# Optimization experiments

Measured on AMD Instinct MI355X. Metric: run time of the kernel, lower is better.

## Reference

```python
import jax, jax.numpy as jnp
import numpy as np
from jax import lax

B, C, H, L = 4, 64, 8, 2048  # batch, per-head channels, heads, sequence length


def setup_inputs() -> dict:
    key = jax.random.key(0)
    ks = jax.random.split(key, 15)

    def p(k, shape, s=0.05):
        return jax.random.normal(k, shape, jnp.float32) * s

    inp = {"x": jax.random.normal(ks[0], (B, C, L), jnp.float32)}
    for i, nm in enumerate(["q", "k", "v"]):
        inp[f"{nm}_dw"] = p(ks[1 + 4 * i], (C, 1, 3))       # depthwise conv weight, groups=C, k=3
        inp[f"{nm}_db"] = p(ks[2 + 4 * i], (C,))
        inp[f"{nm}_pw"] = p(ks[3 + 4 * i], (H * C, C))      # pointwise 1x1 conv weight
        inp[f"{nm}_pb"] = p(ks[4 + 4 * i], (H * C,))
    inp["u_w"] = p(ks[13], (C, H * C))                      # unify_heads 1x1 conv weight
    inp["u_b"] = p(ks[14], (C,))
    return inp


def dsconv(x, dw, db, pw, pb):
    # Depth-separable conv1d: depthwise (k=3, pad=1, groups=C) then pointwise 1x1.
    c = x.shape[1]
    y = lax.conv_general_dilated(x, dw, window_strides=(1,), padding=[(1, 1)],
                                 dimension_numbers=("NCH", "OIH", "NCH"),
                                 feature_group_count=c)
    y = y + db[None, :, None]
    return jnp.einsum("bcl,oc->bol", y, pw) + pb[None, :, None]


def reference(x, q_dw, q_db, q_pw, q_pb, k_dw, k_db, k_pw, k_pb,
              v_dw, v_db, v_pw, v_pb, u_w, u_b):
    b, c, l = x.shape
    h = H
    scale = c ** (-0.25)
    q = dsconv(x, q_dw, q_db, q_pw, q_pb).reshape(b, h, c, l) * scale
    k = dsconv(x, k_dw, k_db, k_pw, k_pb).reshape(b, h, c, l) * scale
    v = dsconv(x, v_dw, v_db, v_pw, v_pb).reshape(b, h, c, l)
    # dot[b,h,i,j] = sum_c k[b,h,c,i] * q[b,h,c,j]  (i = key pos, j = query pos)
    dot = jnp.einsum("bhci,bhcj->bhij", k, q)
    att = jax.nn.softmax(dot, axis=2)  # normalize over key positions (torch dim=1 of [bh,l,l])
    out = jnp.einsum("bhci,bhij->bhcj", v, att).reshape(b, h * c, l)
    return jnp.einsum("bkl,ck->bcl", out, u_w) + u_b[None, :, None]
```

## Files before the change

### kernel.cpp

```cpp
#include <hip/hip_runtime.h>
#include <hip/hip_bf16.h>
#include <stdint.h>
#include <string.h>

typedef unsigned short u16;
typedef unsigned int u32;
typedef __bf16 bf16x8 __attribute__((ext_vector_type(8)));
typedef float f32x4 __attribute__((ext_vector_type(4)));

#define NB 4
#define NC 64
#define NH 8
#define NL 2048
#define HC 512

#define XT_OFF  ((size_t)0)
#define WM_OFF  ((size_t)1 << 20)
#define PBM_OFF ((size_t)2 << 20)
#define V_OFF   ((size_t)4 << 20)
#define QT_OFF  ((size_t)12 << 20)
#define KT_OFF  ((size_t)20 << 20)

#define LP 72

#if __has_builtin(__builtin_amdgcn_exp2f)
#define EXP2F __builtin_amdgcn_exp2f
#else
#define EXP2F exp2f
#endif

static __device__ __forceinline__ u16 f2bfu(float f) {
  union { float f; unsigned int i; } x; x.f = f;
  unsigned int i = x.i;
  return (u16)((i + 0x7fffu + ((i >> 16) & 1u)) >> 16);
}
static __device__ __forceinline__ u32 pk2(float a, float b) {
  float2 f; f.x = a; f.y = b;
  __hip_bfloat162 h = __float22bfloat162_rn(f);
  u32 w; __builtin_memcpy(&w, &h, 4); return w;
}
static __device__ __forceinline__ bf16x8 ld_bf8(const u16* p) {
  bf16x8 v; __builtin_memcpy(&v, p, 16); return v;
}

__global__ __launch_bounds__(256) void init_out(
    const float* __restrict__ ub, float* __restrict__ out)
{
  int i4 = blockIdx.x * 256 + threadIdx.x;
  int c = (i4 >> 9) & 63;
  float f = ub[c];
  float4 v = {f, f, f, f};
  ((float4*)out)[i4] = v;
}

__global__ __launch_bounds__(256) void prep_w(
    const float* __restrict__ qdw, const float* __restrict__ qdb,
    const float* __restrict__ qpw, const float* __restrict__ qpb,
    const float* __restrict__ kdw, const float* __restrict__ kdb,
    const float* __restrict__ kpw, const float* __restrict__ kpb,
    const float* __restrict__ vdw, const float* __restrict__ vdb,
    const float* __restrict__ vpw, const float* __restrict__ vpb,
    u16* __restrict__ Wm, float* __restrict__ pbm)
{
  int idx = blockIdx.x * 256 + threadIdx.x;
  if (idx < 98304) {
    int tns = idx >> 15, r = idx & 32767, o = r >> 6, c = r & 63;
    const float* dw = (tns == 0) ? qdw : (tns == 1) ? kdw : vdw;
    const float* pw = (tns == 0) ? qpw : (tns == 1) ? kpw : vpw;
    float s = (tns == 0) ? 0.35355339059327373f * 1.4426950408889634f
            : (tns == 1) ? 0.35355339059327373f : 1.0f;
    float w = pw[o * 64 + c] * s;
#pragma unroll
    for (int d = 0; d < 3; ++d)
      Wm[((size_t)(tns * 3 + d) * 512 + o) * 64 + c] = f2bfu(w * dw[c * 3 + d]);
  } else if (idx < 98304 + 1536) {
    int i = idx - 98304;
    int tns = i >> 9, o = i & 511;
    const float* db = (tns == 0) ? qdb : (tns == 1) ? kdb : vdb;
    const float* pw = (tns == 0) ? qpw : (tns == 1) ? kpw : vpw;
    const float* pb = (tns == 0) ? qpb : (tns == 1) ? kpb : vpb;
    float s = (tns == 0) ? 0.35355339059327373f * 1.4426950408889634f
            : (tns == 1) ? 0.35355339059327373f : 1.0f;
    float bias = pb[o];
    for (int c = 0; c < 64; ++c) bias += pw[o * 64 + c] * db[c];
    pbm[i] = bias * s;
  }
}

__global__ __launch_bounds__(256) void prep_x(
    const float* __restrict__ x, u16* __restrict__ xT)
{
  __shared__ __align__(16) u16 T[64 * LP];
  int bx = blockIdx.x;
  int lt = bx & 31, b = bx >> 5;
  int tid = threadIdx.x;
  {
    int c = tid & 63, ls = (tid >> 6) * 16;
    const float4* g = (const float4*)(x + ((size_t)b * NC + c) * NL + lt * 64 + ls);
    u16 tmp[16];
#pragma unroll
    for (int j4 = 0; j4 < 4; ++j4) {
      float4 f = g[j4];
      tmp[j4*4+0] = f2bfu(f.x); tmp[j4*4+1] = f2bfu(f.y);
      tmp[j4*4+2] = f2bfu(f.z); tmp[j4*4+3] = f2bfu(f.w);
    }
#pragma unroll
    for (int j = 0; j < 16; ++j) T[(ls + j) * LP + c] = tmp[j];
  }
  __syncthreads();
  {
    int r = tid >> 2, cs = (tid & 3) * 16;
    uint4 a = *(const uint4*)&T[r * LP + cs];
    uint4 b2 = *(const uint4*)&T[r * LP + cs + 8];
    u16* o = xT + ((size_t)b * NL + lt * 64 + r) * 64 + cs;
    *(uint4*)o = a;
    *(uint4*)(o + 8) = b2;
  }
}

__global__ __launch_bounds__(256) void qkv_gemm(
    const u16* __restrict__ xT, const u16* __restrict__ Wm,
    const float* __restrict__ pbm,
    u16* __restrict__ v, u16* __restrict__ qT, u16* __restrict__ kT)
{
  __shared__ __align__(16) u16 WS[3][64 * LP];
  __shared__ __align__(16) u16 XS[66 * LP];

  int bx = blockIdx.x;
  int och = bx & 7;
  int tns = (bx >> 3) % 3;
  int rest = bx / 24;
  int lt = rest & 31, b = rest >> 5;

  int tid = threadIdx.x;
  int wave = tid >> 6, lane = tid & 63, quad = lane >> 4, l16 = lane & 15;

  {
    const u16* wg = Wm + ((size_t)(tns * 3) * 512 + och * 64) * 64;
    for (int s = tid; s < 1536; s += 256) {
      int d = s >> 9, r = s & 511;
      int o = r >> 3, c4 = r & 7;
      uint4 w = *(const uint4*)(wg + ((size_t)d * 512 + o) * 64 + c4 * 8);
      *(uint4*)&WS[d][o * LP + c4 * 8] = w;
    }
  }
  {
    const u16* xg = xT + (size_t)b * NL * 64;
    int l0m1 = lt * 64 - 1;
    for (int s = tid; s < 528; s += 256) {
      int r = s >> 3, c4 = s & 7;
      int g = l0m1 + r;
      uint4 w = {0, 0, 0, 0};
      if ((unsigned)g < (unsigned)NL) w = *(const uint4*)(xg + (size_t)g * 64 + c4 * 8);
      *(uint4*)&XS[r * LP + c4 * 8] = w;
    }
  }
  __syncthreads();

  f32x4 acc[4] = {{0,0,0,0},{0,0,0,0},{0,0,0,0},{0,0,0,0}};

  if (tns == 2) {
    bf16x8 aw[3][2];
#pragma unroll
    for (int d = 0; d < 3; ++d)
#pragma unroll
      for (int kh = 0; kh < 2; ++kh)
        aw[d][kh] = ld_bf8(&WS[d][(wave * 16 + l16) * LP + kh * 32 + quad * 8]);
#pragma unroll
    for (int nt = 0; nt < 4; ++nt)
#pragma unroll
      for (int d = 0; d < 3; ++d)
#pragma unroll
        for (int kh = 0; kh < 2; ++kh) {
          bf16x8 bx8 = ld_bf8(&XS[(nt * 16 + l16 + d) * LP + kh * 32 + quad * 8]);
          acc[nt] = __builtin_amdgcn_mfma_f32_16x16x32_bf16(aw[d][kh], bx8, acc[nt], 0, 0, 0);
        }
  } else {
    bf16x8 ax[3][2];
#pragma unroll
    for (int d = 0; d < 3; ++d)
#pragma unroll
      for (int kh = 0; kh < 2; ++kh)
        ax[d][kh] = ld_bf8(&XS[(wave * 16 + l16 + d) * LP + kh * 32 + quad * 8]);
#pragma unroll
    for (int nt = 0; nt < 4; ++nt)
#pragma unroll
      for (int d = 0; d < 3; ++d)
#pragma unroll
        for (int kh = 0; kh < 2; ++kh) {
          bf16x8 bw = ld_bf8(&WS[d][(nt * 16 + l16) * LP + kh * 32 + quad * 8]);
          acc[nt] = __builtin_amdgcn_mfma_f32_16x16x32_bf16(ax[d][kh], bw, acc[nt], 0, 0, 0);
        }
  }

  __syncthreads();
  u16* OS = &WS[0][0];

  if (tns == 2) {
    const float* pbt = pbm + tns * 512 + och * 64 + wave * 16;
#pragma unroll
    for (int nt = 0; nt < 4; ++nt)
#pragma unroll
      for (int rr = 0; rr < 4; ++rr)
        OS[(wave * 16 + quad * 4 + rr) * LP + nt * 16 + l16] =
            f2bfu(acc[nt][rr] + pbt[quad * 4 + rr]);
  } else {
    const float* pbt = pbm + tns * 512 + och * 64;
#pragma unroll
    for (int nt = 0; nt < 4; ++nt) {
      float bias = pbt[nt * 16 + l16];
#pragma unroll
      for (int rr = 0; rr < 4; ++rr)
        OS[(wave * 16 + quad * 4 + rr) * LP + nt * 16 + l16] = f2bfu(acc[nt][rr] + bias);
    }
  }
  __syncthreads();

  {
    int r = tid >> 2, ck = (tid & 3) * 16;
    uint4 a = *(const uint4*)&OS[r * LP + ck];
    uint4 b2 = *(const uint4*)&OS[r * LP + ck + 8];
    u16* gp;
    if (tns == 2)
      gp = v + ((size_t)(b * HC + och * 64 + r)) * NL + lt * 64 + ck;
    else {
      u16* dst = (tns == 0) ? qT : kT;
      gp = dst + ((size_t)(b * 8 + och) * NL + lt * 64 + r) * 64 + ck;
    }
    *(uint4*)gp = a;
    *(uint4*)(gp + 8) = b2;
  }
}

__global__ __launch_bounds__(256) void attn_kernel(
    const u16* __restrict__ qT, const u16* __restrict__ kT,
    const u16* __restrict__ vg, const float* __restrict__ uw,
    float* __restrict__ outg)
{
  __shared__ __align__(16) u16 Kt[64 * LP];
  __shared__ __align__(16) u16 Vt[64 * LP];
  __shared__ __align__(16) u16 UW[64 * LP];
  __shared__ __align__(16) u16 QP[128 * LP];

  int bx = blockIdx.x;
  int qt = bx & 15, bh = bx >> 4;
  int b = bh >> 3, h = bh & 7;
  int tid = threadIdx.x;
  int wave = tid >> 6, lane = tid & 63, quad = lane >> 4, l16 = lane & 15;

  const u16* Qh = qT + (size_t)bh * NL * 64;
  const u16* Kh = kT + (size_t)bh * NL * 64;
  const u16* Vh = vg + ((size_t)(b * HC + h * NC)) * NL;
  int q0 = qt * 128;

  int sr = tid >> 2, ss = (tid & 3) * 16;
  int vc = tid & 63, vk = (tid >> 6) * 16;

  {
    int r = tid >> 1, cs = (tid & 1) * 32;
    const u16* g = Qh + (size_t)(q0 + r) * 64 + cs;
    uint4 a0 = *(const uint4*)g;
    uint4 a1 = *(const uint4*)(g + 8);
    uint4 a2 = *(const uint4*)(g + 16);
    uint4 a3 = *(const uint4*)(g + 24);
    u16* d = &QP[r * LP + cs];
    *(uint4*)d = a0; *(uint4*)(d + 8) = a1;
    *(uint4*)(d + 16) = a2; *(uint4*)(d + 24) = a3;
  }
  {
    int c = tid >> 2, g = (tid & 3) * 16;
    const float4* s = (const float4*)(uw + (size_t)c * HC + h * 64 + g);
#pragma unroll
    for (int j = 0; j < 4; ++j) {
      float4 w = s[j];
      u16* d = &UW[c * LP + g + j * 4];
      d[0] = f2bfu(w.x); d[1] = f2bfu(w.y); d[2] = f2bfu(w.z); d[3] = f2bfu(w.w);
    }
  }
  __syncthreads();

  bf16x8 bq[2][2];
#pragma unroll
  for (int t = 0; t < 2; ++t)
#pragma unroll
    for (int kh = 0; kh < 2; ++kh)
      bq[t][kh] = ld_bf8(&QP[(wave * 32 + t * 16 + l16) * LP + kh * 32 + quad * 8]);

  f32x4 o[2][4];
#pragma unroll
  for (int t = 0; t < 2; ++t)
#pragma unroll
    for (int ct = 0; ct < 4; ++ct) o[t][ct] = (f32x4){0, 0, 0, 0};
  float l_part[2] = {0.f, 0.f};

  uint4 ka, kb, va, vb;
  {
    const u16* ks = Kh + (size_t)sr * 64 + ss;
    ka = *(const uint4*)ks; kb = *(const uint4*)(ks + 8);
    const u16* vs = Vh + (size_t)vc * NL + vk;
    va = *(const uint4*)vs; vb = *(const uint4*)(vs + 8);
  }

  u16* Pw = &QP[wave * 32 * LP];

  for (int kt0 = 0; kt0 < NL; kt0 += 64) {
    __syncthreads();
    *(uint4*)&Kt[sr * LP + ss] = ka;
    *(uint4*)&Kt[sr * LP + ss + 8] = kb;
    *(uint4*)&Vt[vc * LP + vk] = va;
    *(uint4*)&Vt[vc * LP + vk + 8] = vb;
    __syncthreads();
    if (kt0 + 64 < NL) {
      const u16* ks = Kh + (size_t)(kt0 + 64 + sr) * 64 + ss;
      ka = *(const uint4*)ks; kb = *(const uint4*)(ks + 8);
      const u16* vs = Vh + (size_t)vc * NL + kt0 + 64 + vk;
      va = *(const uint4*)vs; vb = *(const uint4*)(vs + 8);
    }

    bf16x8 ak[4][2], av[4][2];
#pragma unroll
    for (int i = 0; i < 4; ++i)
#pragma unroll
      for (int kh = 0; kh < 2; ++kh) {
        ak[i][kh] = ld_bf8(&Kt[(i * 16 + l16) * LP + kh * 32 + quad * 8]);
        av[i][kh] = ld_bf8(&Vt[(i * 16 + l16) * LP + kh * 32 + quad * 8]);
      }

#pragma unroll
    for (int t = 0; t < 2; ++t) {
      f32x4 s[4];
#pragma unroll
      for (int ktl = 0; ktl < 4; ++ktl) {
        f32x4 z = {0, 0, 0, 0};
        z = __builtin_amdgcn_mfma_f32_16x16x32_bf16(ak[ktl][0], bq[t][0], z, 0, 0, 0);
        z = __builtin_amdgcn_mfma_f32_16x16x32_bf16(ak[ktl][1], bq[t][1], z, 0, 0, 0);
        s[ktl] = z;
      }
      u16* Pq = &Pw[(t * 16 + l16) * LP];
#pragma unroll
      for (int ktl = 0; ktl < 4; ++ktl) {
        float p0 = EXP2F(s[ktl][0]);
        float p1 = EXP2F(s[ktl][1]);
        float p2 = EXP2F(s[ktl][2]);
        float p3 = EXP2F(s[ktl][3]);
        l_part[t] += p0 + p1 + p2 + p3;
        *(u32*)&Pq[ktl * 16 + quad * 4] = pk2(p0, p1);
        *(u32*)&Pq[ktl * 16 + quad * 4 + 2] = pk2(p2, p3);
      }
#pragma unroll
      for (int kh = 0; kh < 2; ++kh) {
        bf16x8 bp = ld_bf8(&Pq[kh * 32 + quad * 8]);
#pragma unroll
        for (int ct = 0; ct < 4; ++ct)
          o[t][ct] = __builtin_amdgcn_mfma_f32_16x16x32_bf16(av[ct][kh], bp, o[t][ct], 0, 0, 0);
      }
    }
  }

  float* ob = outg + ((size_t)b * NC) * NL;
#pragma unroll
  for (int t = 0; t < 2; ++t) {
    float lp = l_part[t];
    lp += __shfl_xor(lp, 16);
    lp += __shfl_xor(lp, 32);
    float rinv = 1.0f / lp;
    u16* OT = &Pw[(t * 16 + l16) * LP];
    *(u32*)&OT[ 0 + quad * 4]     = pk2(o[t][0][0]*rinv, o[t][0][1]*rinv);
    *(u32*)&OT[ 0 + quad * 4 + 2] = pk2(o[t][0][2]*rinv, o[t][0][3]*rinv);
    *(u32*)&OT[16 + quad * 4]     = pk2(o[t][1][0]*rinv, o[t][1][1]*rinv);
    *(u32*)&OT[16 + quad * 4 + 2] = pk2(o[t][1][2]*rinv, o[t][1][3]*rinv);
    *(u32*)&OT[32 + quad * 4]     = pk2(o[t][2][0]*rinv, o[t][2][1]*rinv);
    *(u32*)&OT[32 + quad * 4 + 2] = pk2(o[t][2][2]*rinv, o[t][2][3]*rinv);
    *(u32*)&OT[48 + quad * 4]     = pk2(o[t][3][0]*rinv, o[t][3][1]*rinv);
    *(u32*)&OT[48 + quad * 4 + 2] = pk2(o[t][3][2]*rinv, o[t][3][3]*rinv);

    int qcol = q0 + wave * 32 + t * 16 + l16;
#pragma unroll
    for (int mt = 0; mt < 4; ++mt) {
      f32x4 acc = {0, 0, 0, 0};
#pragma unroll
      for (int kh = 0; kh < 2; ++kh) {
        bf16x8 a = ld_bf8(&UW[(mt * 16 + l16) * LP + kh * 32 + quad * 8]);
        bf16x8 bt = ld_bf8(&OT[kh * 32 + quad * 8]);
        acc = __builtin_amdgcn_mfma_f32_16x16x32_bf16(a, bt, acc, 0, 0, 0);
      }
#pragma unroll
      for (int rr = 0; rr < 4; ++rr) {
        int c = mt * 16 + quad * 4 + rr;
        atomicAdd(&ob[(size_t)c * NL + qcol], acc[rr]);
      }
    }
  }
}

extern "C" void kernel_launch(void* const* d_in, const int* in_sizes, int n_in,
                              void* d_out, int out_size, void* d_ws, size_t ws_size,
                              hipStream_t stream) {
  (void)in_sizes; (void)n_in; (void)out_size; (void)ws_size;
  const float* x   = (const float*)d_in[0];
  const float* qdw = (const float*)d_in[1];
  const float* qdb = (const float*)d_in[2];
  const float* qpw = (const float*)d_in[3];
  const float* qpb = (const float*)d_in[4];
  const float* kdw = (const float*)d_in[5];
  const float* kdb = (const float*)d_in[6];
  const float* kpw = (const float*)d_in[7];
  const float* kpb = (const float*)d_in[8];
  const float* vdw = (const float*)d_in[9];
  const float* vdb = (const float*)d_in[10];
  const float* vpw = (const float*)d_in[11];
  const float* vpb = (const float*)d_in[12];
  const float* uw  = (const float*)d_in[13];
  const float* ub  = (const float*)d_in[14];

  char* ws = (char*)d_ws;
  u16*   xT  = (u16*)(ws + XT_OFF);
  u16*   Wm  = (u16*)(ws + WM_OFF);
  float* pbm = (float*)(ws + PBM_OFF);
  u16*   v   = (u16*)(ws + V_OFF);
  u16*   qT  = (u16*)(ws + QT_OFF);
  u16*   kT  = (u16*)(ws + KT_OFF);
  float* out = (float*)d_out;

  init_out<<<512, 256, 0, stream>>>(ub, out);
  prep_w<<<390, 256, 0, stream>>>(
      qdw, qdb, qpw, qpb, kdw, kdb, kpw, kpb, vdw, vdb, vpw, vpb, Wm, pbm);
  prep_x<<<NB * 32, 256, 0, stream>>>(x, xT);
  qkv_gemm<<<NB * 32 * 3 * 8, 256, 0, stream>>>(xT, Wm, pbm, v, qT, kT);
  attn_kernel<<<32 * 16, 256, 0, stream>>>(qT, kT, v, uw, out);
}
```

Baseline: 164.2 us.

## Merge prep kernels, double-buffer attention K/V tiles, and loop qkv_gemm over tiles

Result: faster. 158.9 us (-3.2%).

```diff
diff --git a/kernel.cpp b/kernel.cpp
--- a/kernel.cpp
+++ b/kernel.cpp
@@ -21,7 +21,7 @@
 #define QT_OFF  ((size_t)12 << 20)
 #define KT_OFF  ((size_t)20 << 20)
 
-#define LP 72
+#define LP 68
 
 #if __has_builtin(__builtin_amdgcn_exp2f)
 #define EXP2F __builtin_amdgcn_exp2f
@@ -43,78 +43,81 @@
   bf16x8 v; __builtin_memcpy(&v, p, 16); return v;
 }
 
-__global__ __launch_bounds__(256) void init_out(
-    const float* __restrict__ ub, float* __restrict__ out)
-{
-  int i4 = blockIdx.x * 256 + threadIdx.x;
-  int c = (i4 >> 9) & 63;
-  float f = ub[c];
-  float4 v = {f, f, f, f};
-  ((float4*)out)[i4] = v;
-}
-
-__global__ __launch_bounds__(256) void prep_w(
+__global__ __launch_bounds__(256) void prep_all(
+    const float* __restrict__ x,
     const float* __restrict__ qdw, const float* __restrict__ qdb,
     const float* __restrict__ qpw, const float* __restrict__ qpb,
     const float* __restrict__ kdw, const float* __restrict__ kdb,
     const float* __restrict__ kpw, const float* __restrict__ kpb,
     const float* __restrict__ vdw, const float* __restrict__ vdb,
     const float* __restrict__ vpw, const float* __restrict__ vpb,
-    u16* __restrict__ Wm, float* __restrict__ pbm)
-{
-  int idx = blockIdx.x * 256 + threadIdx.x;
-  if (idx < 98304) {
-    int tns = idx >> 15, r = idx & 32767, o = r >> 6, c = r & 63;
-    const float* dw = (tns == 0) ? qdw : (tns == 1) ? kdw : vdw;
-    const float* pw = (tns == 0) ? qpw : (tns == 1) ? kpw : vpw;
-    float s = (tns == 0) ? 0.35355339059327373f * 1.4426950408889634f
-            : (tns == 1) ? 0.35355339059327373f : 1.0f;
-    float w = pw[o * 64 + c] * s;
-#pragma unroll
-    for (int d = 0; d < 3; ++d)
-      Wm[((size_t)(tns * 3 + d) * 512 + o) * 64 + c] = f2bfu(w * dw[c * 3 + d]);
-  } else if (idx < 98304 + 1536) {
-    int i = idx - 98304;
-    int tns = i >> 9, o = i & 511;
-    const float* db = (tns == 0) ? qdb : (tns == 1) ? kdb : vdb;
-    const float* pw = (tns == 0) ? qpw : (tns == 1) ? kpw : vpw;
-    const float* pb = (tns == 0) ? qpb : (tns == 1) ? kpb : vpb;
-    float s = (tns == 0) ? 0.35355339059327373f * 1.4426950408889634f
-            : (tns == 1) ? 0.35355339059327373f : 1.0f;
-    float bias = pb[o];
-    for (int c = 0; c < 64; ++c) bias += pw[o * 64 + c] * db[c];
-    pbm[i] = bias * s;
-  }
-}
-
-__global__ __launch_bounds__(256) void prep_x(
-    const float* __restrict__ x, u16* __restrict__ xT)
+    const float* __restrict__ ub,
+    u16* __restrict__ Wm, float* __restrict__ pbm,
+    u16* __restrict__ xT, float* __restrict__ out)
 {
   __shared__ __align__(16) u16 T[64 * LP];
   int bx = blockIdx.x;
-  int lt = bx & 31, b = bx >> 5;
   int tid = threadIdx.x;
+
+  if (bx < 512) {
+    int i4 = bx * 256 + tid;
+    int c = (i4 >> 9) & 63;
+    float f = ub[c];
+    float4 v = {f, f, f, f};
+    ((float4*)out)[i4] = v;
+    return;
+  }
+  if (bx < 902) {
+    int idx = (bx - 512) * 256 + tid;
+    if (idx < 98304) {
+      int tns = idx >> 15, r = idx & 32767, o = r >> 6, c = r & 63;
+      const float* dw = (tns == 0) ? qdw : (tns == 1) ? kdw : vdw;
+      const float* pw = (tns == 0) ? qpw : (tns == 1) ? kpw : vpw;
+      float s = (tns == 0) ? 0.35355339059327373f * 1.4426950408889634f
+              : (tns == 1) ? 0.35355339059327373f : 1.0f;
+      float w = pw[o * 64 + c] * s;
+#pragma unroll
+      for (int d = 0; d < 3; ++d)
+        Wm[((size_t)(tns * 3 + d) * 512 + o) * 64 + c] = f2bfu(w * dw[c * 3 + d]);
+    } else {
+      int i = idx - 98304;
+      int tns = i >> 9, o = i & 511;
+      const float* db = (tns == 0) ? qdb : (tns == 1) ? kdb : vdb;
+      const float* pw = (tns == 0) ? qpw : (tns == 1) ? kpw : vpw;
+      const float* pb = (tns == 0) ? qpb : (tns == 1) ? kpb : vpb;
+      float s = (tns == 0) ? 0.35355339059327373f * 1.4426950408889634f
+              : (tns == 1) ? 0.35355339059327373f : 1.0f;
+      float bias = pb[o];
+      for (int c = 0; c < 64; ++c) bias += pw[o * 64 + c] * db[c];
+      pbm[i] = bias * s;
+    }
+    return;
+  }
   {
-    int c = tid & 63, ls = (tid >> 6) * 16;
-    const float4* g = (const float4*)(x + ((size_t)b * NC + c) * NL + lt * 64 + ls);
-    u16 tmp[16];
-#pragma unroll
-    for (int j4 = 0; j4 < 4; ++j4) {
-      float4 f = g[j4];
-      tmp[j4*4+0] = f2bfu(f.x); tmp[j4*4+1] = f2bfu(f.y);
-      tmp[j4*4+2] = f2bfu(f.z); tmp[j4*4+3] = f2bfu(f.w);
-    }
-#pragma unroll
-    for (int j = 0; j < 16; ++j) T[(ls + j) * LP + c] = tmp[j];
-  }
-  __syncthreads();
-  {
-    int r = tid >> 2, cs = (tid & 3) * 16;
-    uint4 a = *(const uint4*)&T[r * LP + cs];
-    uint4 b2 = *(const uint4*)&T[r * LP + cs + 8];
-    u16* o = xT + ((size_t)b * NL + lt * 64 + r) * 64 + cs;
-    *(uint4*)o = a;
-    *(uint4*)(o + 8) = b2;
+    int b2 = bx - 902;
+    int lt = b2 & 31, b = b2 >> 5;
+    {
+      int c = tid & 63, ls = (tid >> 6) * 16;
+      const float4* g = (const float4*)(x + ((size_t)b * NC + c) * NL + lt * 64 + ls);
+      u16 tmp[16];
+#pragma unroll
+      for (int j4 = 0; j4 < 4; ++j4) {
+        float4 f = g[j4];
+        tmp[j4*4+0] = f2bfu(f.x); tmp[j4*4+1] = f2bfu(f.y);
+        tmp[j4*4+2] = f2bfu(f.z); tmp[j4*4+3] = f2bfu(f.w);
+      }
+#pragma unroll
+      for (int j = 0; j < 16; ++j) T[(ls + j) * LP + c] = tmp[j];
+    }
+    __syncthreads();
+    {
+      int r = tid >> 2, cs = (tid & 3) * 16;
+      uint4 a = *(const uint4*)&T[r * LP + cs];
+      uint4 b3 = *(const uint4*)&T[r * LP + cs + 8];
+      u16* o = xT + ((size_t)b * NL + lt * 64 + r) * 64 + cs;
+      *(uint4*)o = a;
+      *(uint4*)(o + 8) = b3;
+    }
   }
 }
 
@@ -124,112 +127,145 @@
     u16* __restrict__ v, u16* __restrict__ qT, u16* __restrict__ kT)
 {
   __shared__ __align__(16) u16 WS[3][64 * LP];
-  __shared__ __align__(16) u16 XS[66 * LP];
+  __shared__ __align__(16) u16 XS[2][66 * LP];
+  __shared__ __align__(16) u16 OS[64 * LP];
 
   int bx = blockIdx.x;
-  int och = bx & 7;
-  int tns = (bx >> 3) % 3;
-  int rest = bx / 24;
-  int lt = rest & 31, b = rest >> 5;
+  int lg  = bx & 7;
+  int och = (bx >> 3) & 7;
+  int tmp = bx >> 6;
+  int tns = tmp % 3;
+  int b   = tmp / 3;
 
   int tid = threadIdx.x;
   int wave = tid >> 6, lane = tid & 63, quad = lane >> 4, l16 = lane & 15;
+  const u16* xg = xT + (size_t)b * NL * 64;
 
   {
     const u16* wg = Wm + ((size_t)(tns * 3) * 512 + och * 64) * 64;
-    for (int s = tid; s < 1536; s += 256) {
+#pragma unroll
+    for (int it = 0; it < 6; ++it) {
+      int s = tid + it * 256;
       int d = s >> 9, r = s & 511;
       int o = r >> 3, c4 = r & 7;
       uint4 w = *(const uint4*)(wg + ((size_t)d * 512 + o) * 64 + c4 * 8);
       *(uint4*)&WS[d][o * LP + c4 * 8] = w;
     }
   }
-  {
-    const u16* xg = xT + (size_t)b * NL * 64;
-    int l0m1 = lt * 64 - 1;
-    for (int s = tid; s < 528; s += 256) {
-      int r = s >> 3, c4 = s & 7;
-      int g = l0m1 + r;
-      uint4 w = {0, 0, 0, 0};
-      if ((unsigned)g < (unsigned)NL) w = *(const uint4*)(xg + (size_t)g * 64 + c4 * 8);
-      *(uint4*)&XS[r * LP + c4 * 8] = w;
-    }
-  }
+
+  int xr0 = tid >> 3,          xc0 = (tid & 7) * 8;
+  int xr1 = (tid + 256) >> 3,  xc1 = xc0;
+  int xr2 = (tid + 512) >> 3,  xc2 = xc0;
+  uint4 R0, R1, R2;
+  uint4 Z = {0, 0, 0, 0};
+
+#define LOAD_XS(tt)                                                         \
+  {                                                                         \
+    int base = (lg * 4 + (tt)) * 64 - 1;                                    \
+    int g0 = base + xr0, g1 = base + xr1, g2 = base + xr2;                  \
+    R0 = ((unsigned)g0 < NL) ? *(const uint4*)(xg + (size_t)g0 * 64 + xc0) : Z; \
+    R1 = ((unsigned)g1 < NL) ? *(const uint4*)(xg + (size_t)g1 * 64 + xc1) : Z; \
+    if (tid < 16)                                                           \
+      R2 = ((unsigned)g2 < NL) ? *(const uint4*)(xg + (size_t)g2 * 64 + xc2) : Z; \
+  }
+#define STORE_XS(bf)                                                        \
+  {                                                                         \
+    *(uint4*)&XS[bf][xr0 * LP + xc0] = R0;                                  \
+    *(uint4*)&XS[bf][xr1 * LP + xc1] = R1;                                  \
+    if (tid < 16) *(uint4*)&XS[bf][xr2 * LP + xc2] = R2;                    \
+  }
+
+  LOAD_XS(0); STORE_XS(0);
+  LOAD_XS(1);
   __syncthreads();
 
-  f32x4 acc[4] = {{0,0,0,0},{0,0,0,0},{0,0,0,0},{0,0,0,0}};
-
+  float bias4[4];
+  bf16x8 aw[3][2];
   if (tns == 2) {
-    bf16x8 aw[3][2];
+    const float* pbt = pbm + tns * 512 + och * 64 + wave * 16;
+#pragma unroll
+    for (int rr = 0; rr < 4; ++rr) bias4[rr] = pbt[quad * 4 + rr];
 #pragma unroll
     for (int d = 0; d < 3; ++d)
 #pragma unroll
       for (int kh = 0; kh < 2; ++kh)
         aw[d][kh] = ld_bf8(&WS[d][(wave * 16 + l16) * LP + kh * 32 + quad * 8]);
-#pragma unroll
-    for (int nt = 0; nt < 4; ++nt)
-#pragma unroll
-      for (int d = 0; d < 3; ++d)
-#pragma unroll
-        for (int kh = 0; kh < 2; ++kh) {
-          bf16x8 bx8 = ld_bf8(&XS[(nt * 16 + l16 + d) * LP + kh * 32 + quad * 8]);
-          acc[nt] = __builtin_amdgcn_mfma_f32_16x16x32_bf16(aw[d][kh], bx8, acc[nt], 0, 0, 0);
-        }
-  } else {
-    bf16x8 ax[3][2];
-#pragma unroll
-    for (int d = 0; d < 3; ++d)
-#pragma unroll
-      for (int kh = 0; kh < 2; ++kh)
-        ax[d][kh] = ld_bf8(&XS[(wave * 16 + l16 + d) * LP + kh * 32 + quad * 8]);
-#pragma unroll
-    for (int nt = 0; nt < 4; ++nt)
-#pragma unroll
-      for (int d = 0; d < 3; ++d)
-#pragma unroll
-        for (int kh = 0; kh < 2; ++kh) {
-          bf16x8 bw = ld_bf8(&WS[d][(nt * 16 + l16) * LP + kh * 32 + quad * 8]);
-          acc[nt] = __builtin_amdgcn_mfma_f32_16x16x32_bf16(ax[d][kh], bw, acc[nt], 0, 0, 0);
-        }
-  }
-
-  __syncthreads();
-  u16* OS = &WS[0][0];
-
-  if (tns == 2) {
-    const float* pbt = pbm + tns * 512 + och * 64 + wave * 16;
-#pragma unroll
-    for (int nt = 0; nt < 4; ++nt)
-#pragma unroll
-      for (int rr = 0; rr < 4; ++rr)
-        OS[(wave * 16 + quad * 4 + rr) * LP + nt * 16 + l16] =
-            f2bfu(acc[nt][rr] + pbt[quad * 4 + rr]);
   } else {
     const float* pbt = pbm + tns * 512 + och * 64;
 #pragma unroll
-    for (int nt = 0; nt < 4; ++nt) {
-      float bias = pbt[nt * 16 + l16];
-#pragma unroll
-      for (int rr = 0; rr < 4; ++rr)
-        OS[(wave * 16 + quad * 4 + rr) * LP + nt * 16 + l16] = f2bfu(acc[nt][rr] + bias);
-    }
-  }
-  __syncthreads();
-
-  {
-    int r = tid >> 2, ck = (tid & 3) * 16;
-    uint4 a = *(const uint4*)&OS[r * LP + ck];
-    uint4 b2 = *(const uint4*)&OS[r * LP + ck + 8];
-    u16* gp;
-    if (tns == 2)
-      gp = v + ((size_t)(b * HC + och * 64 + r)) * NL + lt * 64 + ck;
-    else {
-      u16* dst = (tns == 0) ? qT : kT;
-      gp = dst + ((size_t)(b * 8 + och) * NL + lt * 64 + r) * 64 + ck;
-    }
-    *(uint4*)gp = a;
-    *(uint4*)(gp + 8) = b2;
-  }
+    for (int nt = 0; nt < 4; ++nt) bias4[nt] = pbt[nt * 16 + l16];
+  }
+
+  for (int t = 0; t < 4; ++t) {
+    int cur = t & 1;
+    f32x4 acc[4] = {{0,0,0,0},{0,0,0,0},{0,0,0,0},{0,0,0,0}};
+
+    if (tns == 2) {
+#pragma unroll
+      for (int nt = 0; nt < 4; ++nt)
+#pragma unroll
+        for (int d = 0; d < 3; ++d)
+#pragma unroll
+          for (int kh = 0; kh < 2; ++kh) {
+            bf16x8 bx8 = ld_bf8(&XS[cur][(nt * 16 + l16 + d) * LP + kh * 32 + quad * 8]);
+            acc[nt] = __builtin_amdgcn_mfma_f32_16x16x32_bf16(aw[d][kh], bx8, acc[nt], 0, 0, 0);
+          }
+    } else {
+      bf16x8 ax[3][2];
+#pragma unroll
+      for (int d = 0; d < 3; ++d)
+#pragma unroll
+        for (int kh = 0; kh < 2; ++kh)
+          ax[d][kh] = ld_bf8(&XS[cur][(wave * 16 + l16 + d) * LP + kh * 32 + quad * 8]);
+#pragma unroll
+      for (int nt = 0; nt < 4; ++nt)
+#pragma unroll
+        for (int d = 0; d < 3; ++d)
+#pragma unroll
+          for (int kh = 0; kh < 2; ++kh) {
+            bf16x8 bw = ld_bf8(&WS[d][(nt * 16 + l16) * LP + kh * 32 + quad * 8]);
+            acc[nt] = __builtin_amdgcn_mfma_f32_16x16x32_bf16(ax[d][kh], bw, acc[nt], 0, 0, 0);
+          }
+    }
+
+    if (t < 3) { STORE_XS((t + 1) & 1); if (t < 2) LOAD_XS(t + 2); }
+    __syncthreads();
+
+    if (tns == 2) {
+#pragma unroll
+      for (int nt = 0; nt < 4; ++nt)
+#pragma unroll
+        for (int rr = 0; rr < 4; ++rr)
+          OS[(wave * 16 + quad * 4 + rr) * LP + nt * 16 + l16] =
+              f2bfu(acc[nt][rr] + bias4[rr]);
+    } else {
+#pragma unroll
+      for (int nt = 0; nt < 4; ++nt)
+#pragma unroll
+        for (int rr = 0; rr < 4; ++rr)
+          OS[(wave * 16 + quad * 4 + rr) * LP + nt * 16 + l16] =
+              f2bfu(acc[nt][rr] + bias4[nt]);
+    }
+    __syncthreads();
+
+    {
+      int lt = lg * 4 + t;
+      int r = tid >> 2, ck = (tid & 3) * 16;
+      uint4 a = *(const uint4*)&OS[r * LP + ck];
+      uint4 b2 = *(const uint4*)&OS[r * LP + ck + 8];
+      u16* gp;
+      if (tns == 2)
+        gp = v + ((size_t)(b * HC + och * 64 + r)) * NL + lt * 64 + ck;
+      else {
+        u16* dst = (tns == 0) ? qT : kT;
+        gp = dst + ((size_t)(b * 8 + och) * NL + lt * 64 + r) * 64 + ck;
+      }
+      *(uint4*)gp = a;
+      *(uint4*)(gp + 8) = b2;
+    }
+  }
+#undef LOAD_XS
+#undef STORE_XS
 }
 
 __global__ __launch_bounds__(256) void attn_kernel(
@@ -237,8 +273,8 @@
     const u16* __restrict__ vg, const float* __restrict__ uw,
     float* __restrict__ outg)
 {
-  __shared__ __align__(16) u16 Kt[64 * LP];
-  __shared__ __align__(16) u16 Vt[64 * LP];
+  __shared__ __align__(16) u16 Kt[2][64 * LP];
+  __shared__ __align__(16) u16 Vt[2][64 * LP];
   __shared__ __align__(16) u16 UW[64 * LP];
   __shared__ __align__(16) u16 QP[128 * LP];
 
@@ -277,21 +313,6 @@
       d[0] = f2bfu(w.x); d[1] = f2bfu(w.y); d[2] = f2bfu(w.z); d[3] = f2bfu(w.w);
     }
   }
-  __syncthreads();
-
-  bf16x8 bq[2][2];
-#pragma unroll
-  for (int t = 0; t < 2; ++t)
-#pragma unroll
-    for (int kh = 0; kh < 2; ++kh)
-      bq[t][kh] = ld_bf8(&QP[(wave * 32 + t * 16 + l16) * LP + kh * 32 + quad * 8]);
-
-  f32x4 o[2][4];
-#pragma unroll
-  for (int t = 0; t < 2; ++t)
-#pragma unroll
-    for (int ct = 0; ct < 4; ++ct) o[t][ct] = (f32x4){0, 0, 0, 0};
-  float l_part[2] = {0.f, 0.f};
 
   uint4 ka, kb, va, vb;
   {
@@ -299,31 +320,42 @@
     ka = *(const uint4*)ks; kb = *(const uint4*)(ks + 8);
     const u16* vs = Vh + (size_t)vc * NL + vk;
     va = *(const uint4*)vs; vb = *(const uint4*)(vs + 8);
-  }
+    *(uint4*)&Kt[0][sr * LP + ss] = ka;
+    *(uint4*)&Kt[0][sr * LP + ss + 8] = kb;
+    *(uint4*)&Vt[0][vc * LP + vk] = va;
+    *(uint4*)&Vt[0][vc * LP + vk + 8] = vb;
+    const u16* ks1 = Kh + (size_t)(64 + sr) * 64 + ss;
+    ka = *(const uint4*)ks1; kb = *(const uint4*)(ks1 + 8);
+    const u16* vs1 = Vh + (size_t)vc * NL + 64 + vk;
+    va = *(const uint4*)vs1; vb = *(const uint4*)(vs1 + 8);
+  }
+  __syncthreads();
+
+  bf16x8 bq[2][2];
+#pragma unroll
+  for (int t = 0; t < 2; ++t)
+#pragma unroll
+    for (int kh = 0; kh < 2; ++kh)
+      bq[t][kh] = ld_bf8(&QP[(wave * 32 + t * 16 + l16) * LP + kh * 32 + quad * 8]);
+
+  f32x4 o[2][4];
+#pragma unroll
+  for (int t = 0; t < 2; ++t)
+#pragma unroll
+    for (int ct = 0; ct < 4; ++ct) o[t][ct] = (f32x4){0, 0, 0, 0};
+  float l_part[2] = {0.f, 0.f};
 
   u16* Pw = &QP[wave * 32 * LP];
 
-  for (int kt0 = 0; kt0 < NL; kt0 += 64) {
-    __syncthreads();
-    *(uint4*)&Kt[sr * LP + ss] = ka;
-    *(uint4*)&Kt[sr * LP + ss + 8] = kb;
-    *(uint4*)&Vt[vc * LP + vk] = va;
-    *(uint4*)&Vt[vc * LP + vk + 8] = vb;
-    __syncthreads();
-    if (kt0 + 64 < NL) {
-      const u16* ks = Kh + (size_t)(kt0 + 64 + sr) * 64 + ss;
-      ka = *(const uint4*)ks; kb = *(const uint4*)(ks + 8);
-      const u16* vs = Vh + (size_t)vc * NL + kt0 + 64 + vk;
-      va = *(const uint4*)vs; vb = *(const uint4*)(vs + 8);
-    }
-
+  for (int i = 0; i < 32; ++i) {
+    int cur = i & 1;
     bf16x8 ak[4][2], av[4][2];
 #pragma unroll
-    for (int i = 0; i < 4; ++i)
+    for (int j = 0; j < 4; ++j)
 #pragma unroll
       for (int kh = 0; kh < 2; ++kh) {
-        ak[i][kh] = ld_bf8(&Kt[(i * 16 + l16) * LP + kh * 32 + quad * 8]);
-        av[i][kh] = ld_bf8(&Vt[(i * 16 + l16) * LP + kh * 32 + quad * 8]);
+        ak[j][kh] = ld_bf8(&Kt[cur][(j * 16 + l16) * LP + kh * 32 + quad * 8]);
+        av[j][kh] = ld_bf8(&Vt[cur][(j * 16 + l16) * LP + kh * 32 + quad * 8]);
       }
 
 #pragma unroll
@@ -355,6 +387,22 @@
           o[t][ct] = __builtin_amdgcn_mfma_f32_16x16x32_bf16(av[ct][kh], bp, o[t][ct], 0, 0, 0);
       }
     }
+
+    if (i < 31) {
+      int nxt = cur ^ 1;
+      *(uint4*)&Kt[nxt][sr * LP + ss] = ka;
+      *(uint4*)&Kt[nxt][sr * LP + ss + 8] = kb;
+      *(uint4*)&Vt[nxt][vc * LP + vk] = va;
+      *(uint4*)&Vt[nxt][vc * LP + vk + 8] = vb;
+      if (i < 30) {
+        int kt2 = (i + 2) * 64;
+        const u16* ks = Kh + (size_t)(kt2 + sr) * 64 + ss;
+        ka = *(const uint4*)ks; kb = *(const uint4*)(ks + 8);
+        const u16* vs = Vh + (size_t)vc * NL + kt2 + vk;
+        va = *(const uint4*)vs; vb = *(const uint4*)(vs + 8);
+      }
+    }
+    __syncthreads();
   }
 
   float* ob = outg + ((size_t)b * NC) * NL;
@@ -422,10 +470,9 @@
   u16*   kT  = (u16*)(ws + KT_OFF);
   float* out = (float*)d_out;
 
-  init_out<<<512, 256, 0, stream>>>(ub, out);
-  prep_w<<<390, 256, 0, stream>>>(
-      qdw, qdb, qpw, qpb, kdw, kdb, kpw, kpb, vdw, vdb, vpw, vpb, Wm, pbm);
-  prep_x<<<NB * 32, 256, 0, stream>>>(x, xT);
-  qkv_gemm<<<NB * 32 * 3 * 8, 256, 0, stream>>>(xT, Wm, pbm, v, qT, kT);
-  attn_kernel<<<32 * 16, 256, 0, stream>>>(qT, kT, v, uw, out);
-}
+  prep_all<<<1030, 256, 0, stream>>>(
+      x, qdw, qdb, qpw, qpb, kdw, kdb, kpw, kpb, vdw, vdb, vpw, vpb,
+      ub, Wm, pbm, xT, out);
+  qkv_gemm<<<768, 256, 0, stream>>>(xT, Wm, pbm, v, qT, kT);
+  attn_kernel<<<512, 256, 0, stream>>>(qT, kT, v, uw, out);
+}
```
